# Kernel tuning notes

Measured on AMD Instinct MI355X. Metric: run time of the kernel, lower is better.

The kernel has to match this reference:

```python
import jax, jax.numpy as jnp
import numpy as np

B = 8192
DIM_Q = 1024
DIM_U = 1024
NUM_CHARTS = 16
TOP_K = 2


def setup_inputs() -> dict:
    key = jax.random.key(0)
    k1, k2, k3 = jax.random.split(key, 3)
    q = jax.random.normal(k1, (B, DIM_Q), dtype=jnp.float32)
    weights = jax.random.uniform(k2, (B, NUM_CHARTS), dtype=jnp.float32)
    # W_stack init: -I + 0.01*randn per chart (dim_q == dim_u branch)
    W_stack = (-jnp.eye(DIM_Q, dtype=jnp.float32)[None, :, :]
               + 0.01 * jax.random.normal(k3, (NUM_CHARTS, DIM_U, DIM_Q), dtype=jnp.float32))
    return {"q": q, "weights": weights, "W_stack": W_stack}


def reference(q, weights, W_stack):
    # Top-k gated mixture of linear maps: out[b] = sum_{c in topk(weights[b])} w_norm[b,c] * W_stack[c] @ q[b]
    b = q.shape[0]
    w_vals, idx = jax.lax.top_k(weights, TOP_K)              # [B, k], sorted descending (matches torch.topk)
    w_norm = w_vals / jnp.clip(jnp.sum(w_vals, axis=1, keepdims=True), 1e-8, None)
    # scatter normalized weights back to dense [B, num_charts] gate matrix
    w_masked = jnp.zeros_like(weights).at[jnp.arange(b)[:, None], idx].set(w_norm)
    out = jnp.zeros((b, W_stack.shape[1]), dtype=q.dtype)
    for c in range(NUM_CHARTS):  # small fixed expert count
        out = out + w_masked[:, c:c + 1] * (q @ W_stack[c].T)  # [B, dim_u]
    return out
```

## Files before the change

kernel.cpp:

```cpp
#include <hip/hip_runtime.h>
#include <hip/hip_bf16.h>
#include <stdint.h>

#define NROWS 8192
#define DIMQ 1024
#define DIMU 1024
#define NCH 16

#define BM 128
#define BN 128
#define BK 64

typedef __attribute__((ext_vector_type(4))) float f32x4;
typedef __attribute__((ext_vector_type(8))) short bf16x8;

__device__ __forceinline__ short f2bf(float f) {
    union { __hip_bfloat16 h; short s; } u;
    u.h = __float2bfloat16(f);
    return u.s;
}

__global__ void cvt2_kernel(const float* __restrict__ q, const float* __restrict__ Ws,
                            short* __restrict__ qb, short* __restrict__ Wb) {
    const int nq = NROWS * DIMQ / 8;
    const int nw = NCH * DIMU * DIMQ / 8;
    int i0 = blockIdx.x * blockDim.x + threadIdx.x;
    int stride = gridDim.x * blockDim.x;
    for (int i = i0; i < nq; i += stride) {
        const f32x4* p = reinterpret_cast<const f32x4*>(q + (size_t)i * 8);
        f32x4 a = p[0], b = p[1];
        bf16x8 o;
        o[0] = f2bf(a[0]); o[1] = f2bf(a[1]); o[2] = f2bf(a[2]); o[3] = f2bf(a[3]);
        o[4] = f2bf(b[0]); o[5] = f2bf(b[1]); o[6] = f2bf(b[2]); o[7] = f2bf(b[3]);
        *reinterpret_cast<bf16x8*>(qb + (size_t)i * 8) = o;
    }
    for (int i = i0; i < nw; i += stride) {
        const f32x4* p = reinterpret_cast<const f32x4*>(Ws + (size_t)i * 8);
        f32x4 a = p[0], b = p[1];
        bf16x8 o;
        o[0] = f2bf(a[0]); o[1] = f2bf(a[1]); o[2] = f2bf(a[2]); o[3] = f2bf(a[3]);
        o[4] = f2bf(b[0]); o[5] = f2bf(b[1]); o[6] = f2bf(b[2]); o[7] = f2bf(b[3]);
        *reinterpret_cast<bf16x8*>(Wb + (size_t)i * 8) = o;
    }
}

__global__ void gate_kernel(const float* __restrict__ weights,
                            int* __restrict__ cnt,
                            int* __restrict__ rowlist,
                            float* __restrict__ wgt) {
    __shared__ int lcnt[NCH];
    __shared__ int lbase[NCH];
    const int t = threadIdx.x;
    const int b = blockIdx.x * blockDim.x + t;
    if (t < NCH) lcnt[t] = 0;
    __syncthreads();

    float w[NCH];
    const f32x4* wp = reinterpret_cast<const f32x4*>(weights + (size_t)b * NCH);
#pragma unroll
    for (int i = 0; i < 4; ++i) {
        f32x4 v = wp[i];
        w[i * 4 + 0] = v[0]; w[i * 4 + 1] = v[1];
        w[i * 4 + 2] = v[2]; w[i * 4 + 3] = v[3];
    }
    int i0 = 0; float v0 = w[0];
#pragma unroll
    for (int i = 1; i < NCH; ++i) if (w[i] > v0) { v0 = w[i]; i0 = i; }
    int i1 = (i0 == 0) ? 1 : 0; float v1 = w[i1];
#pragma unroll
    for (int i = 0; i < NCH; ++i) if (i != i0 && w[i] > v1) { v1 = w[i]; i1 = i; }
    float s = v0 + v1;
    s = (s < 1e-8f) ? 1e-8f : s;
    float n0 = v0 / s, n1 = v1 / s;

    int p0 = atomicAdd(&lcnt[i0], 1);
    int p1 = atomicAdd(&lcnt[i1], 1);
    __syncthreads();
    if (t < NCH) lbase[t] = atomicAdd(&cnt[t], lcnt[t]);
    __syncthreads();

    int o0 = lbase[i0] + p0;
    int o1 = lbase[i1] + p1;
    rowlist[(size_t)i0 * NROWS + o0] = b;  wgt[(size_t)i0 * NROWS + o0] = n0;
    rowlist[(size_t)i1 * NROWS + o1] = b;  wgt[(size_t)i1 * NROWS + o1] = n1;
}

__global__ __launch_bounds__(256, 3) void moe_gemm_bf(
    const short* __restrict__ qb, const short* __restrict__ Wb,
    const int* __restrict__ cnt, const int* __restrict__ rowlist,
    const float* __restrict__ wgt, float* __restrict__ out)
{
    const int id  = blockIdx.x;
    const int xcd = id & 7;
    const int k   = id >> 3;
    const int c   = xcd + ((k >> 9) << 3);
    const int kk  = k & 511;
    const int n0  = (kk & 7) * BN;
    const int m0  = (kk >> 3) * BM;

    const int count = cnt[c];
    if (m0 >= count) return;

    __shared__ short sA[BM * BK];
    __shared__ short sB[BN * BK];
    __shared__ int   sRow[BM];
    __shared__ float sW[BM];

    const int t = threadIdx.x;
    if (t < BM) {
        int gi = m0 + t;
        int r = 0; float wv_ = 0.f;
        if (gi < count) {
            r   = rowlist[(size_t)c * NROWS + gi];
            wv_ = wgt[(size_t)c * NROWS + gi];
        }
        sRow[t] = r; sW[t] = wv_;
    }
    __syncthreads();

    const short* aSrc[4];
    const short* bSrc[4];
#pragma unroll
    for (int i = 0; i < 4; ++i) {
        int ch = i * 256 + t;
        int r  = ch >> 3;
        int c8 = ch & 7;
        aSrc[i] = qb + (size_t)sRow[r] * DIMQ + c8 * 8;
        bSrc[i] = Wb + (size_t)c * ((size_t)DIMU * DIMQ) + (size_t)(n0 + r) * DIMQ + c8 * 8;
    }

    const int lane = t & 63;
    const int wv   = t >> 6;
    const int wm   = (wv >> 1) * 64;
    const int wn   = (wv & 1) * 64;
    const int rr   = lane & 15;
    const int g    = lane >> 4;

    f32x4 acc[4][4];
#pragma unroll
    for (int r = 0; r < 4; ++r)
#pragma unroll
        for (int cc = 0; cc < 4; ++cc)
            acc[r][cc] = (f32x4){0.f, 0.f, 0.f, 0.f};

    const int NKT = DIMQ / BK;
    for (int kt = 0; kt < NKT; ++kt) {
        __syncthreads();
#pragma unroll
        for (int i = 0; i < 4; ++i)
            __builtin_amdgcn_global_load_lds(aSrc[i] + kt * BK, &sA[(i * 256 + t) * 8], 16, 0, 0);
#pragma unroll
        for (int i = 0; i < 4; ++i)
            __builtin_amdgcn_global_load_lds(bSrc[i] + kt * BK, &sB[(i * 256 + t) * 8], 16, 0, 0);
        __syncthreads();

#pragma unroll
        for (int ks = 0; ks < 2; ++ks) {
            bf16x8 af[4], bfr[4];
#pragma unroll
            for (int r = 0; r < 4; ++r) {
                af[r]  = *reinterpret_cast<const bf16x8*>(&sA[(wm + r * 16 + rr) * BK + ks * 32 + g * 8]);
                bfr[r] = *reinterpret_cast<const bf16x8*>(&sB[(wn + r * 16 + rr) * BK + ks * 32 + g * 8]);
            }
#pragma unroll
            for (int r = 0; r < 4; ++r)
#pragma unroll
                for (int cc = 0; cc < 4; ++cc)
                    acc[r][cc] = __builtin_amdgcn_mfma_f32_16x16x32_bf16(af[r], bfr[cc], acc[r][cc], 0, 0, 0);
        }
    }

#pragma unroll
    for (int r = 0; r < 4; ++r) {
#pragma unroll
        for (int cc = 0; cc < 4; ++cc) {
#pragma unroll
            for (int j = 0; j < 4; ++j) {
                int rowInTile = wm + r * 16 + g * 4 + j;
                int gi = m0 + rowInTile;
                if (gi < count) {
                    int   orow = sRow[rowInTile];
                    float wgx  = sW[rowInTile];
                    int   col  = n0 + wn + cc * 16 + rr;
                    atomicAdd(&out[(size_t)orow * DIMU + col], acc[r][cc][j] * wgx);
                }
            }
        }
    }
}

#define BKF 32
#define LDSTRF 40
typedef __attribute__((ext_vector_type(4))) short s16x4;

__global__ __launch_bounds__(256, 2) void moe_gemm_f32(
    const float* __restrict__ q, const float* __restrict__ Wst,
    const int* __restrict__ cnt, const int* __restrict__ rowlist,
    const float* __restrict__ wgt, float* __restrict__ out)
{
    const int c  = blockIdx.z;
    const int n0 = blockIdx.x * BN;
    const int m0 = blockIdx.y * BM;
    const int count = cnt[c];
    if (m0 >= count) return;

    __shared__ short sA[BM * LDSTRF];
    __shared__ short sB[BN * LDSTRF];
    __shared__ int   sRow[BM];
    __shared__ float sW[BM];

    const int t = threadIdx.x;
    if (t < BM) {
        int gi = m0 + t;
        int r = 0; float w = 0.f;
        if (gi < count) {
            r = rowlist[(size_t)c * NROWS + gi];
            w = wgt[(size_t)c * NROWS + gi];
        }
        sRow[t] = r; sW[t] = w;
    }
    __syncthreads();

    const float* aBase[4];
    const float* bBase[4];
    int ldsOff[4];
#pragma unroll
    for (int i = 0; i < 4; ++i) {
        int f  = t + i * 256;
        int r  = f >> 3;
        int c4 = f & 7;
        aBase[i]  = q   + (size_t)sRow[r] * DIMQ + c4 * 4;
        bBase[i]  = Wst + (size_t)c * ((size_t)DIMU * DIMQ) + (size_t)(n0 + r) * DIMQ + c4 * 4;
        ldsOff[i] = r * LDSTRF + c4 * 4;
    }

    const int lane = t & 63;
    const int wv   = t >> 6;
    const int wm   = (wv >> 1) * 64;
    const int wn   = (wv & 1) * 64;
    const int rr   = lane & 15;
    const int g    = lane >> 4;

    f32x4 acc[4][4];
#pragma unroll
    for (int r = 0; r < 4; ++r)
#pragma unroll
        for (int cc = 0; cc < 4; ++cc)
            acc[r][cc] = (f32x4){0.f, 0.f, 0.f, 0.f};

    f32x4 pa[4], pb[4];
#pragma unroll
    for (int i = 0; i < 4; ++i) {
        pa[i] = *reinterpret_cast<const f32x4*>(aBase[i]);
        pb[i] = *reinterpret_cast<const f32x4*>(bBase[i]);
    }

    const int NKT = DIMQ / BKF;
    for (int kt = 0; kt < NKT; ++kt) {
        __syncthreads();
#pragma unroll
        for (int i = 0; i < 4; ++i) {
            s16x4 va, vb;
#pragma unroll
            for (int j = 0; j < 4; ++j) { va[j] = f2bf(pa[i][j]); vb[j] = f2bf(pb[i][j]); }
            *reinterpret_cast<s16x4*>(&sA[ldsOff[i]]) = va;
            *reinterpret_cast<s16x4*>(&sB[ldsOff[i]]) = vb;
        }
        __syncthreads();

        if (kt + 1 < NKT) {
            int k = (kt + 1) * BKF;
#pragma unroll
            for (int i = 0; i < 4; ++i) {
                pa[i] = *reinterpret_cast<const f32x4*>(aBase[i] + k);
                pb[i] = *reinterpret_cast<const f32x4*>(bBase[i] + k);
            }
        }

        bf16x8 af[4], bfr[4];
#pragma unroll
        for (int r = 0; r < 4; ++r) {
            af[r]  = *reinterpret_cast<const bf16x8*>(&sA[(wm + r * 16 + rr) * LDSTRF + g * 8]);
            bfr[r] = *reinterpret_cast<const bf16x8*>(&sB[(wn + r * 16 + rr) * LDSTRF + g * 8]);
        }
#pragma unroll
        for (int r = 0; r < 4; ++r)
#pragma unroll
            for (int cc = 0; cc < 4; ++cc)
                acc[r][cc] = __builtin_amdgcn_mfma_f32_16x16x32_bf16(af[r], bfr[cc], acc[r][cc], 0, 0, 0);
    }

#pragma unroll
    for (int r = 0; r < 4; ++r) {
#pragma unroll
        for (int cc = 0; cc < 4; ++cc) {
#pragma unroll
            for (int j = 0; j < 4; ++j) {
                int rowInTile = wm + r * 16 + g * 4 + j;
                int gi = m0 + rowInTile;
                if (gi < count) {
                    int   orow = sRow[rowInTile];
                    float w    = sW[rowInTile];
                    int   col  = n0 + wn + cc * 16 + rr;
                    atomicAdd(&out[(size_t)orow * DIMU + col], acc[r][cc][j] * w);
                }
            }
        }
    }
}

extern "C" void kernel_launch(void* const* d_in, const int* in_sizes, int n_in,
                              void* d_out, int out_size, void* d_ws, size_t ws_size,
                              hipStream_t stream) {
    const float* q  = (const float*)d_in[0];
    const float* w  = (const float*)d_in[1];
    const float* Ws = (const float*)d_in[2];
    float* out = (float*)d_out;

    const size_t qbf_bytes  = (size_t)NROWS * DIMQ * 2;
    const size_t wbf_bytes  = (size_t)NCH * DIMU * (size_t)DIMQ * 2;
    const size_t meta_bytes = 256 + (size_t)NCH * NROWS * (sizeof(int) + sizeof(float));
    char* ws = (char*)d_ws;

    if (ws_size >= qbf_bytes + wbf_bytes + meta_bytes) {
        short* qb      = (short*)ws;
        short* Wb      = (short*)(ws + qbf_bytes);
        int*   cnt     = (int*)(ws + qbf_bytes + wbf_bytes);
        int*   rowlist = (int*)(ws + qbf_bytes + wbf_bytes + 256);
        float* wgt     = (float*)(ws + qbf_bytes + wbf_bytes + 256 + (size_t)NCH * NROWS * sizeof(int));

        hipMemsetAsync(cnt, 0, 256, stream);
        hipMemsetAsync(d_out, 0, (size_t)out_size * sizeof(float), stream);

        cvt2_kernel<<<2048, 256, 0, stream>>>(q, Ws, qb, Wb);
        gate_kernel<<<NROWS / 256, 256, 0, stream>>>(w, cnt, rowlist, wgt);

        moe_gemm_bf<<<8192, 256, 0, stream>>>(qb, Wb, cnt, rowlist, wgt, out);
    } else {
        int*   cnt     = (int*)ws;
        int*   rowlist = (int*)(ws + 256);
        float* wgt     = (float*)(ws + 256 + (size_t)NCH * NROWS * sizeof(int));

        hipMemsetAsync(cnt, 0, 256, stream);
        hipMemsetAsync(d_out, 0, (size_t)out_size * sizeof(float), stream);

        gate_kernel<<<NROWS / 256, 256, 0, stream>>>(w, cnt, rowlist, wgt);

        dim3 grid(DIMU / BN, NROWS / BM, NCH);
        moe_gemm_f32<<<grid, 256, 0, stream>>>(q, Ws, cnt, rowlist, wgt, out);
    }
}
```

Measured before the change: 241.1 us.

## Use persistent M-slot loop with register-prefetched global loads and padded LDS

Replaces the 8192-block grid, where most blocks exit early, with 2048 blocks that each loop over M tiles of one chart in strides of 16 slots. Global-to-LDS direct loads become register prefetches of the next K tile, issued while MFMAs run on the current tile. LDS rows are padded to a stride of 72 to cut bank conflicts. The trade-offs are higher register pressure and the loss of the async LDS load path, and chart load imbalance now falls on fewer, longer-running blocks.

```diff
diff --git a/kernel.cpp b/kernel.cpp
--- a/kernel.cpp
+++ b/kernel.cpp
@@ -10,8 +10,11 @@
 #define BM 128
 #define BN 128
 #define BK 64
+#define LDSTR 72
+#define MSLOTS 16
 
 typedef __attribute__((ext_vector_type(4))) float f32x4;
+typedef __attribute__((ext_vector_type(4))) short s16x4;
 typedef __attribute__((ext_vector_type(8))) short bf16x8;
 
 __device__ __forceinline__ short f2bf(float f) {
@@ -90,45 +93,21 @@
     const int* __restrict__ cnt, const int* __restrict__ rowlist,
     const float* __restrict__ wgt, float* __restrict__ out)
 {
-    const int id  = blockIdx.x;
-    const int xcd = id & 7;
-    const int k   = id >> 3;
-    const int c   = xcd + ((k >> 9) << 3);
-    const int kk  = k & 511;
-    const int n0  = (kk & 7) * BN;
-    const int m0  = (kk >> 3) * BM;
+    const int id    = blockIdx.x;
+    const int xcd   = id & 7;
+    const int rest  = id >> 3;
+    const int c     = xcd + 8 * (rest & 1);
+    const int n0    = ((rest >> 1) & 7) * BN;
+    const int mslot = rest >> 4;
 
     const int count = cnt[c];
-    if (m0 >= count) return;
-
-    __shared__ short sA[BM * BK];
-    __shared__ short sB[BN * BK];
+
+    __shared__ short sA[BM * LDSTR];
+    __shared__ short sB[BN * LDSTR];
     __shared__ int   sRow[BM];
     __shared__ float sW[BM];
 
-    const int t = threadIdx.x;
-    if (t < BM) {
-        int gi = m0 + t;
-        int r = 0; float wv_ = 0.f;
-        if (gi < count) {
-            r   = rowlist[(size_t)c * NROWS + gi];
-            wv_ = wgt[(size_t)c * NROWS + gi];
-        }
-        sRow[t] = r; sW[t] = wv_;
-    }
-    __syncthreads();
-
-    const short* aSrc[4];
-    const short* bSrc[4];
-#pragma unroll
-    for (int i = 0; i < 4; ++i) {
-        int ch = i * 256 + t;
-        int r  = ch >> 3;
-        int c8 = ch & 7;
-        aSrc[i] = qb + (size_t)sRow[r] * DIMQ + c8 * 8;
-        bSrc[i] = Wb + (size_t)c * ((size_t)DIMU * DIMQ) + (size_t)(n0 + r) * DIMQ + c8 * 8;
-    }
-
+    const int t    = threadIdx.x;
     const int lane = t & 63;
     const int wv   = t >> 6;
     const int wm   = (wv >> 1) * 64;
@@ -136,53 +115,95 @@
     const int rr   = lane & 15;
     const int g    = lane >> 4;
 
-    f32x4 acc[4][4];
-#pragma unroll
-    for (int r = 0; r < 4; ++r)
-#pragma unroll
-        for (int cc = 0; cc < 4; ++cc)
-            acc[r][cc] = (f32x4){0.f, 0.f, 0.f, 0.f};
-
-    const int NKT = DIMQ / BK;
-    for (int kt = 0; kt < NKT; ++kt) {
+    for (int m0 = mslot * BM; m0 < count; m0 += MSLOTS * BM) {
         __syncthreads();
-#pragma unroll
-        for (int i = 0; i < 4; ++i)
-            __builtin_amdgcn_global_load_lds(aSrc[i] + kt * BK, &sA[(i * 256 + t) * 8], 16, 0, 0);
-#pragma unroll
-        for (int i = 0; i < 4; ++i)
-            __builtin_amdgcn_global_load_lds(bSrc[i] + kt * BK, &sB[(i * 256 + t) * 8], 16, 0, 0);
+        if (t < BM) {
+            int gi = m0 + t;
+            int r = 0; float wv_ = 0.f;
+            if (gi < count) {
+                r   = rowlist[(size_t)c * NROWS + gi];
+                wv_ = wgt[(size_t)c * NROWS + gi];
+            }
+            sRow[t] = r; sW[t] = wv_;
+        }
         __syncthreads();
 
-#pragma unroll
-        for (int ks = 0; ks < 2; ++ks) {
-            bf16x8 af[4], bfr[4];
-#pragma unroll
-            for (int r = 0; r < 4; ++r) {
-                af[r]  = *reinterpret_cast<const bf16x8*>(&sA[(wm + r * 16 + rr) * BK + ks * 32 + g * 8]);
-                bfr[r] = *reinterpret_cast<const bf16x8*>(&sB[(wn + r * 16 + rr) * BK + ks * 32 + g * 8]);
-            }
-#pragma unroll
-            for (int r = 0; r < 4; ++r)
-#pragma unroll
-                for (int cc = 0; cc < 4; ++cc)
-                    acc[r][cc] = __builtin_amdgcn_mfma_f32_16x16x32_bf16(af[r], bfr[cc], acc[r][cc], 0, 0, 0);
-        }
-    }
-
-#pragma unroll
-    for (int r = 0; r < 4; ++r) {
-#pragma unroll
-        for (int cc = 0; cc < 4; ++cc) {
-#pragma unroll
-            for (int j = 0; j < 4; ++j) {
-                int rowInTile = wm + r * 16 + g * 4 + j;
-                int gi = m0 + rowInTile;
-                if (gi < count) {
-                    int   orow = sRow[rowInTile];
-                    float wgx  = sW[rowInTile];
-                    int   col  = n0 + wn + cc * 16 + rr;
-                    atomicAdd(&out[(size_t)orow * DIMU + col], acc[r][cc][j] * wgx);
+        const short* aSrc[4];
+        const short* bSrc[4];
+        int ldsO[4];
+#pragma unroll
+        for (int i = 0; i < 4; ++i) {
+            int ch = i * 256 + t;
+            int r  = ch >> 3;
+            int c8 = ch & 7;
+            aSrc[i] = qb + (size_t)sRow[r] * DIMQ + c8 * 8;
+            bSrc[i] = Wb + (size_t)c * ((size_t)DIMU * DIMQ) + (size_t)(n0 + r) * DIMQ + c8 * 8;
+            ldsO[i] = r * LDSTR + c8 * 8;
+        }
+
+        f32x4 acc[4][4];
+#pragma unroll
+        for (int r = 0; r < 4; ++r)
+#pragma unroll
+            for (int cc = 0; cc < 4; ++cc)
+                acc[r][cc] = (f32x4){0.f, 0.f, 0.f, 0.f};
+
+        bf16x8 pa[4], pb[4];
+#pragma unroll
+        for (int i = 0; i < 4; ++i) {
+            pa[i] = *reinterpret_cast<const bf16x8*>(aSrc[i]);
+            pb[i] = *reinterpret_cast<const bf16x8*>(bSrc[i]);
+        }
+
+        const int NKT = DIMQ / BK;
+        for (int kt = 0; kt < NKT; ++kt) {
+            __syncthreads();
+#pragma unroll
+            for (int i = 0; i < 4; ++i) {
+                *reinterpret_cast<bf16x8*>(&sA[ldsO[i]]) = pa[i];
+                *reinterpret_cast<bf16x8*>(&sB[ldsO[i]]) = pb[i];
+            }
+            __syncthreads();
+
+            if (kt + 1 < NKT) {
+                int k = (kt + 1) * BK;
+#pragma unroll
+                for (int i = 0; i < 4; ++i) {
+                    pa[i] = *reinterpret_cast<const bf16x8*>(aSrc[i] + k);
+                    pb[i] = *reinterpret_cast<const bf16x8*>(bSrc[i] + k);
+                }
+            }
+
+#pragma unroll
+            for (int ks = 0; ks < 2; ++ks) {
+                bf16x8 af[4], bfr[4];
+#pragma unroll
+                for (int r = 0; r < 4; ++r) {
+                    af[r]  = *reinterpret_cast<const bf16x8*>(&sA[(wm + r * 16 + rr) * LDSTR + ks * 32 + g * 8]);
+                    bfr[r] = *reinterpret_cast<const bf16x8*>(&sB[(wn + r * 16 + rr) * LDSTR + ks * 32 + g * 8]);
+                }
+#pragma unroll
+                for (int r = 0; r < 4; ++r)
+#pragma unroll
+                    for (int cc = 0; cc < 4; ++cc)
+                        acc[r][cc] = __builtin_amdgcn_mfma_f32_16x16x32_bf16(af[r], bfr[cc], acc[r][cc], 0, 0, 0);
+            }
+        }
+
+#pragma unroll
+        for (int r = 0; r < 4; ++r) {
+#pragma unroll
+            for (int cc = 0; cc < 4; ++cc) {
+#pragma unroll
+                for (int j = 0; j < 4; ++j) {
+                    int rowInTile = wm + r * 16 + g * 4 + j;
+                    int gi = m0 + rowInTile;
+                    if (gi < count) {
+                        int   orow = sRow[rowInTile];
+                        float wgx  = sW[rowInTile];
+                        int   col  = n0 + wn + cc * 16 + rr;
+                        atomicAdd(&out[(size_t)orow * DIMU + col], acc[r][cc][j] * wgx);
+                    }
                 }
             }
         }
@@ -191,7 +212,6 @@
 
 #define BKF 32
 #define LDSTRF 40
-typedef __attribute__((ext_vector_type(4))) short s16x4;
 
 __global__ __launch_bounds__(256, 2) void moe_gemm_f32(
     const float* __restrict__ q, const float* __restrict__ Wst,
@@ -335,7 +355,7 @@
         cvt2_kernel<<<2048, 256, 0, stream>>>(q, Ws, qb, Wb);
         gate_kernel<<<NROWS / 256, 256, 0, stream>>>(w, cnt, rowlist, wgt);
 
-        moe_gemm_bf<<<8192, 256, 0, stream>>>(qb, Wb, cnt, rowlist, wgt, out);
+        moe_gemm_bf<<<2048, 256, 0, stream>>>(qb, Wb, cnt, rowlist, wgt, out);
     } else {
         int*   cnt     = (int*)ws;
         int*   rowlist = (int*)(ws + 256);
```

After: 227.8 us. 5.5% less time.

## Fuse q bf16 conversion into GEMM with register-prefetched padded LDS staging

Applied to the files above, without the earlier changes.

Drops the separate pass that converts q to bf16. The GEMM now reads fp32 q rows directly, converts them in registers and writes them to LDS. Global-to-LDS direct loads are replaced by a register prefetch of the next K tile, and LDS rows are padded to avoid bank conflicts. The XCD-aware block swizzle is replaced by a plain 3D grid. This trades the q conversion traffic for twice the A-tile global read bytes per block, plus extra conversion ALU work and register pressure inside the GEMM.

```diff
diff --git a/kernel.cpp b/kernel.cpp
--- a/kernel.cpp
+++ b/kernel.cpp
@@ -10,8 +10,10 @@
 #define BM 128
 #define BN 128
 #define BK 64
+#define LDSTR 72
 
 typedef __attribute__((ext_vector_type(4))) float f32x4;
+typedef __attribute__((ext_vector_type(4))) short s16x4;
 typedef __attribute__((ext_vector_type(8))) short bf16x8;
 
 __device__ __forceinline__ short f2bf(float f) {
@@ -20,21 +22,11 @@
     return u.s;
 }
 
-__global__ void cvt2_kernel(const float* __restrict__ q, const float* __restrict__ Ws,
-                            short* __restrict__ qb, short* __restrict__ Wb) {
-    const int nq = NROWS * DIMQ / 8;
+__global__ void cvtW_kernel(const float* __restrict__ Ws, short* __restrict__ Wb) {
     const int nw = NCH * DIMU * DIMQ / 8;
-    int i0 = blockIdx.x * blockDim.x + threadIdx.x;
+    int i = blockIdx.x * blockDim.x + threadIdx.x;
     int stride = gridDim.x * blockDim.x;
-    for (int i = i0; i < nq; i += stride) {
-        const f32x4* p = reinterpret_cast<const f32x4*>(q + (size_t)i * 8);
-        f32x4 a = p[0], b = p[1];
-        bf16x8 o;
-        o[0] = f2bf(a[0]); o[1] = f2bf(a[1]); o[2] = f2bf(a[2]); o[3] = f2bf(a[3]);
-        o[4] = f2bf(b[0]); o[5] = f2bf(b[1]); o[6] = f2bf(b[2]); o[7] = f2bf(b[3]);
-        *reinterpret_cast<bf16x8*>(qb + (size_t)i * 8) = o;
-    }
-    for (int i = i0; i < nw; i += stride) {
+    for (; i < nw; i += stride) {
         const f32x4* p = reinterpret_cast<const f32x4*>(Ws + (size_t)i * 8);
         f32x4 a = p[0], b = p[1];
         bf16x8 o;
@@ -86,23 +78,18 @@
 }
 
 __global__ __launch_bounds__(256, 3) void moe_gemm_bf(
-    const short* __restrict__ qb, const short* __restrict__ Wb,
+    const float* __restrict__ q, const short* __restrict__ Wb,
     const int* __restrict__ cnt, const int* __restrict__ rowlist,
     const float* __restrict__ wgt, float* __restrict__ out)
 {
-    const int id  = blockIdx.x;
-    const int xcd = id & 7;
-    const int k   = id >> 3;
-    const int c   = xcd + ((k >> 9) << 3);
-    const int kk  = k & 511;
-    const int n0  = (kk & 7) * BN;
-    const int m0  = (kk >> 3) * BM;
-
+    const int c  = blockIdx.z;
+    const int n0 = blockIdx.x * BN;
+    const int m0 = blockIdx.y * BM;
     const int count = cnt[c];
     if (m0 >= count) return;
 
-    __shared__ short sA[BM * BK];
-    __shared__ short sB[BN * BK];
+    __shared__ short sA[BM * LDSTR];
+    __shared__ short sB[BN * LDSTR];
     __shared__ int   sRow[BM];
     __shared__ float sW[BM];
 
@@ -118,15 +105,25 @@
     }
     __syncthreads();
 
-    const short* aSrc[4];
+    const float* aSrc[8];
+    int aO[8];
+#pragma unroll
+    for (int i = 0; i < 8; ++i) {
+        int ch = i * 256 + t;
+        int r  = ch >> 4;
+        int q4 = ch & 15;
+        aSrc[i] = q + (size_t)sRow[r] * DIMQ + q4 * 4;
+        aO[i]   = r * LDSTR + q4 * 4;
+    }
     const short* bSrc[4];
+    int bO[4];
 #pragma unroll
     for (int i = 0; i < 4; ++i) {
         int ch = i * 256 + t;
         int r  = ch >> 3;
         int c8 = ch & 7;
-        aSrc[i] = qb + (size_t)sRow[r] * DIMQ + c8 * 8;
         bSrc[i] = Wb + (size_t)c * ((size_t)DIMU * DIMQ) + (size_t)(n0 + r) * DIMQ + c8 * 8;
+        bO[i]   = r * LDSTR + c8 * 8;
     }
 
     const int lane = t & 63;
@@ -143,24 +140,43 @@
         for (int cc = 0; cc < 4; ++cc)
             acc[r][cc] = (f32x4){0.f, 0.f, 0.f, 0.f};
 
+    f32x4  pa[8];
+    bf16x8 pb[4];
+#pragma unroll
+    for (int i = 0; i < 8; ++i) pa[i] = *reinterpret_cast<const f32x4*>(aSrc[i]);
+#pragma unroll
+    for (int i = 0; i < 4; ++i) pb[i] = *reinterpret_cast<const bf16x8*>(bSrc[i]);
+
     const int NKT = DIMQ / BK;
     for (int kt = 0; kt < NKT; ++kt) {
         __syncthreads();
 #pragma unroll
+        for (int i = 0; i < 8; ++i) {
+            s16x4 va;
+#pragma unroll
+            for (int j = 0; j < 4; ++j) va[j] = f2bf(pa[i][j]);
+            *reinterpret_cast<s16x4*>(&sA[aO[i]]) = va;
+        }
+#pragma unroll
         for (int i = 0; i < 4; ++i)
-            __builtin_amdgcn_global_load_lds(aSrc[i] + kt * BK, &sA[(i * 256 + t) * 8], 16, 0, 0);
-#pragma unroll
-        for (int i = 0; i < 4; ++i)
-            __builtin_amdgcn_global_load_lds(bSrc[i] + kt * BK, &sB[(i * 256 + t) * 8], 16, 0, 0);
+            *reinterpret_cast<bf16x8*>(&sB[bO[i]]) = pb[i];
         __syncthreads();
+
+        if (kt + 1 < NKT) {
+            int k = (kt + 1) * BK;
+#pragma unroll
+            for (int i = 0; i < 8; ++i) pa[i] = *reinterpret_cast<const f32x4*>(aSrc[i] + k);
+#pragma unroll
+            for (int i = 0; i < 4; ++i) pb[i] = *reinterpret_cast<const bf16x8*>(bSrc[i] + k);
+        }
 
 #pragma unroll
         for (int ks = 0; ks < 2; ++ks) {
             bf16x8 af[4], bfr[4];
 #pragma unroll
             for (int r = 0; r < 4; ++r) {
-                af[r]  = *reinterpret_cast<const bf16x8*>(&sA[(wm + r * 16 + rr) * BK + ks * 32 + g * 8]);
-                bfr[r] = *reinterpret_cast<const bf16x8*>(&sB[(wn + r * 16 + rr) * BK + ks * 32 + g * 8]);
+                af[r]  = *reinterpret_cast<const bf16x8*>(&sA[(wm + r * 16 + rr) * LDSTR + ks * 32 + g * 8]);
+                bfr[r] = *reinterpret_cast<const bf16x8*>(&sB[(wn + r * 16 + rr) * LDSTR + ks * 32 + g * 8]);
             }
 #pragma unroll
             for (int r = 0; r < 4; ++r)
@@ -191,7 +207,6 @@
 
 #define BKF 32
 #define LDSTRF 40
-typedef __attribute__((ext_vector_type(4))) short s16x4;
 
 __global__ __launch_bounds__(256, 2) void moe_gemm_f32(
     const float* __restrict__ q, const float* __restrict__ Wst,
@@ -317,25 +332,24 @@
     const float* Ws = (const float*)d_in[2];
     float* out = (float*)d_out;
 
-    const size_t qbf_bytes  = (size_t)NROWS * DIMQ * 2;
     const size_t wbf_bytes  = (size_t)NCH * DIMU * (size_t)DIMQ * 2;
     const size_t meta_bytes = 256 + (size_t)NCH * NROWS * (sizeof(int) + sizeof(float));
     char* ws = (char*)d_ws;
 
-    if (ws_size >= qbf_bytes + wbf_bytes + meta_bytes) {
-        short* qb      = (short*)ws;
-        short* Wb      = (short*)(ws + qbf_bytes);
-        int*   cnt     = (int*)(ws + qbf_bytes + wbf_bytes);
-        int*   rowlist = (int*)(ws + qbf_bytes + wbf_bytes + 256);
-        float* wgt     = (float*)(ws + qbf_bytes + wbf_bytes + 256 + (size_t)NCH * NROWS * sizeof(int));
+    if (ws_size >= wbf_bytes + meta_bytes) {
+        short* Wb      = (short*)ws;
+        int*   cnt     = (int*)(ws + wbf_bytes);
+        int*   rowlist = (int*)(ws + wbf_bytes + 256);
+        float* wgt     = (float*)(ws + wbf_bytes + 256 + (size_t)NCH * NROWS * sizeof(int));
 
         hipMemsetAsync(cnt, 0, 256, stream);
         hipMemsetAsync(d_out, 0, (size_t)out_size * sizeof(float), stream);
 
-        cvt2_kernel<<<2048, 256, 0, stream>>>(q, Ws, qb, Wb);
+        cvtW_kernel<<<2048, 256, 0, stream>>>(Ws, Wb);
         gate_kernel<<<NROWS / 256, 256, 0, stream>>>(w, cnt, rowlist, wgt);
 
-        moe_gemm_bf<<<8192, 256, 0, stream>>>(qb, Wb, cnt, rowlist, wgt, out);
+        dim3 grid(DIMU / BN, NROWS / BM, NCH);
+        moe_gemm_bf<<<grid, 256, 0, stream>>>(q, Wb, cnt, rowlist, wgt, out);
     } else {
         int*   cnt     = (int*)ws;
         int*   rowlist = (int*)(ws + 256);
```

After: 247.0 us. 2.4% more time.

## Double-buffer LDS tiles with XOR swizzle in bf16 MoE GEMM

Applied to the files above, without the earlier changes.

Adds double-buffered LDS tiles so the global-to-LDS loads for the next K step are issued while MFMAs run on the current buffer, which removes one barrier per iteration. It also XOR-swizzles 16-byte chunks within each row to cut LDS bank conflicts on fragment reads. The XCD-aware linear block mapping is replaced by a plain 3D grid, and launch bounds drop to 2 blocks per CU because LDS use doubles. Occupancy is lower and chart-to-XCD locality is lost. The prefetch is also issued without an explicit wait before the end-of-iteration barrier, so correctness depends on the compiler inserting vmcnt waits.

```diff
diff --git a/kernel.cpp b/kernel.cpp
--- a/kernel.cpp
+++ b/kernel.cpp
@@ -12,6 +12,7 @@
 #define BK 64
 
 typedef __attribute__((ext_vector_type(4))) float f32x4;
+typedef __attribute__((ext_vector_type(4))) short s16x4;
 typedef __attribute__((ext_vector_type(8))) short bf16x8;
 
 __device__ __forceinline__ short f2bf(float f) {
@@ -85,24 +86,19 @@
     rowlist[(size_t)i1 * NROWS + o1] = b;  wgt[(size_t)i1 * NROWS + o1] = n1;
 }
 
-__global__ __launch_bounds__(256, 3) void moe_gemm_bf(
+__global__ __launch_bounds__(256, 2) void moe_gemm_bf(
     const short* __restrict__ qb, const short* __restrict__ Wb,
     const int* __restrict__ cnt, const int* __restrict__ rowlist,
     const float* __restrict__ wgt, float* __restrict__ out)
 {
-    const int id  = blockIdx.x;
-    const int xcd = id & 7;
-    const int k   = id >> 3;
-    const int c   = xcd + ((k >> 9) << 3);
-    const int kk  = k & 511;
-    const int n0  = (kk & 7) * BN;
-    const int m0  = (kk >> 3) * BM;
-
+    const int c  = blockIdx.z;
+    const int n0 = blockIdx.x * BN;
+    const int m0 = blockIdx.y * BM;
     const int count = cnt[c];
     if (m0 >= count) return;
 
-    __shared__ short sA[BM * BK];
-    __shared__ short sB[BN * BK];
+    __shared__ short sA[2][BM * BK];
+    __shared__ short sB[2][BN * BK];
     __shared__ int   sRow[BM];
     __shared__ float sW[BM];
 
@@ -118,15 +114,18 @@
     }
     __syncthreads();
 
-    const short* aSrc[4];
-    const short* bSrc[4];
+    const short* aS[4];
+    const short* bS[4];
+    int ldsO[4];
 #pragma unroll
     for (int i = 0; i < 4; ++i) {
-        int ch = i * 256 + t;
-        int r  = ch >> 3;
-        int c8 = ch & 7;
-        aSrc[i] = qb + (size_t)sRow[r] * DIMQ + c8 * 8;
-        bSrc[i] = Wb + (size_t)c * ((size_t)DIMU * DIMQ) + (size_t)(n0 + r) * DIMQ + c8 * 8;
+        int ch  = i * 256 + t;
+        int r   = ch >> 3;
+        int c16 = ch & 7;
+        int cs  = (c16 ^ (r & 7)) * 8;
+        aS[i]   = qb + (size_t)sRow[r] * DIMQ + cs;
+        bS[i]   = Wb + (size_t)c * ((size_t)DIMU * DIMQ) + (size_t)(n0 + r) * DIMQ + cs;
+        ldsO[i] = ch * 8;
     }
 
     const int lane = t & 63;
@@ -143,24 +142,44 @@
         for (int cc = 0; cc < 4; ++cc)
             acc[r][cc] = (f32x4){0.f, 0.f, 0.f, 0.f};
 
+    int rowA[4], rowB[4];
+#pragma unroll
+    for (int r = 0; r < 4; ++r) {
+        rowA[r] = wm + r * 16 + rr;
+        rowB[r] = wn + r * 16 + rr;
+    }
+
     const int NKT = DIMQ / BK;
+
+#pragma unroll
+    for (int i = 0; i < 4; ++i)
+        __builtin_amdgcn_global_load_lds(aS[i], &sA[0][ldsO[i]], 16, 0, 0);
+#pragma unroll
+    for (int i = 0; i < 4; ++i)
+        __builtin_amdgcn_global_load_lds(bS[i], &sB[0][ldsO[i]], 16, 0, 0);
+    __syncthreads();
+
+    int cur = 0;
     for (int kt = 0; kt < NKT; ++kt) {
-        __syncthreads();
-#pragma unroll
-        for (int i = 0; i < 4; ++i)
-            __builtin_amdgcn_global_load_lds(aSrc[i] + kt * BK, &sA[(i * 256 + t) * 8], 16, 0, 0);
-#pragma unroll
-        for (int i = 0; i < 4; ++i)
-            __builtin_amdgcn_global_load_lds(bSrc[i] + kt * BK, &sB[(i * 256 + t) * 8], 16, 0, 0);
-        __syncthreads();
+        if (kt + 1 < NKT) {
+            int kof = (kt + 1) * BK;
+#pragma unroll
+            for (int i = 0; i < 4; ++i)
+                __builtin_amdgcn_global_load_lds(aS[i] + kof, &sA[cur ^ 1][ldsO[i]], 16, 0, 0);
+#pragma unroll
+            for (int i = 0; i < 4; ++i)
+                __builtin_amdgcn_global_load_lds(bS[i] + kof, &sB[cur ^ 1][ldsO[i]], 16, 0, 0);
+        }
 
 #pragma unroll
         for (int ks = 0; ks < 2; ++ks) {
             bf16x8 af[4], bfr[4];
 #pragma unroll
             for (int r = 0; r < 4; ++r) {
-                af[r]  = *reinterpret_cast<const bf16x8*>(&sA[(wm + r * 16 + rr) * BK + ks * 32 + g * 8]);
-                bfr[r] = *reinterpret_cast<const bf16x8*>(&sB[(wn + r * 16 + rr) * BK + ks * 32 + g * 8]);
+                int oA = (ks * 32 + g * 8) ^ ((rowA[r] & 7) * 8);
+                int oB = (ks * 32 + g * 8) ^ ((rowB[r] & 7) * 8);
+                af[r]  = *reinterpret_cast<const bf16x8*>(&sA[cur][rowA[r] * BK + oA]);
+                bfr[r] = *reinterpret_cast<const bf16x8*>(&sB[cur][rowB[r] * BK + oB]);
             }
 #pragma unroll
             for (int r = 0; r < 4; ++r)
@@ -168,6 +187,9 @@
                 for (int cc = 0; cc < 4; ++cc)
                     acc[r][cc] = __builtin_amdgcn_mfma_f32_16x16x32_bf16(af[r], bfr[cc], acc[r][cc], 0, 0, 0);
         }
+
+        __syncthreads();
+        cur ^= 1;
     }
 
 #pragma unroll
@@ -191,7 +213,6 @@
 
 #define BKF 32
 #define LDSTRF 40
-typedef __attribute__((ext_vector_type(4))) short s16x4;
 
 __global__ __launch_bounds__(256, 2) void moe_gemm_f32(
     const float* __restrict__ q, const float* __restrict__ Wst,
@@ -335,7 +356,8 @@
         cvt2_kernel<<<2048, 256, 0, stream>>>(q, Ws, qb, Wb);
         gate_kernel<<<NROWS / 256, 256, 0, stream>>>(w, cnt, rowlist, wgt);
 
-        moe_gemm_bf<<<8192, 256, 0, stream>>>(qb, Wb, cnt, rowlist, wgt, out);
+        dim3 grid(DIMU / BN, NROWS / BM, NCH);
+        moe_gemm_bf<<<grid, 256, 0, stream>>>(qb, Wb, cnt, rowlist, wgt, out);
     } else {
         int*   cnt     = (int*)ws;
         int*   rowlist = (int*)(ws + 256);
```

Result: slower. 246.0 us (+2.0%).
